# Performance work log

Measured on AMD Instinct MI355X. Metric: run time of the kernel, lower is better.

Reference implementation:

```python
import jax, jax.numpy as jnp
import numpy as np

N = 65536      # nodes (256x256 grid)
E = 1048576    # edges (avg degree 16)
T_IN = 10      # TIME_STEPS_IN
L = 64         # LATENT_DIMS
MID = 128      # LATENT_DIMS * MLP_RATIO
GD = 2         # grid dims


def _lin_init(key, fan_in, fan_out):
    kw, kb = jax.random.split(key)
    s = 1.0 / np.sqrt(fan_in)
    W = jax.random.uniform(kw, (fan_in, fan_out), jnp.float32, -s, s)
    b = jax.random.uniform(kb, (fan_out,), jnp.float32, -s, s)
    return W, b


def setup_inputs() -> dict:
    key = jax.random.key(0)
    ks = jax.random.split(key, 10)
    x = jax.random.normal(ks[0], (N, T_IN), jnp.float32)
    grid = jax.random.uniform(ks[1], (N, GD), jnp.float32)
    edge_index = jax.random.randint(ks[2], (2, E), 0, N, jnp.int64)
    W_proj1, b_proj1 = _lin_init(ks[3], T_IN + GD, MID)
    W_proj2, b_proj2 = _lin_init(ks[4], MID, L)
    Wk, bk = _lin_init(ks[5], 2 * L + 2 * GD + 1, L)   # K edge MLP (single linear)
    Ww, bw = _lin_init(ks[6], L, L)                     # W node MLP (single linear)
    W_dec1, b_dec1 = _lin_init(ks[7], L, MID)
    W_dec2, b_dec2 = _lin_init(ks[8], MID, 1)
    return {"x": x, "grid": grid, "edge_index": edge_index,
            "W_proj1": W_proj1, "b_proj1": b_proj1, "W_proj2": W_proj2, "b_proj2": b_proj2,
            "Wk": Wk, "bk": bk, "Ww": Ww, "bw": bw,
            "W_dec1": W_dec1, "b_dec1": b_dec1, "W_dec2": W_dec2, "b_dec2": b_dec2}


def _gelu(x):
    return jax.nn.gelu(x, approximate=False)  # torch F.gelu default = exact erf


def reference(x, grid, edge_index, W_proj1, b_proj1, W_proj2, b_proj2,
              Wk, bk, Ww, bw, W_dec1, b_dec1, W_dec2, b_dec2):
    # project: cat(x, grid) -> Linear -> GELU -> Linear
    h = jnp.concatenate([x, grid], axis=-1)               # [N, T_IN+2]
    h = _gelu(h @ W_proj1 + b_proj1) @ W_proj2 + b_proj2  # [N, L]

    # message passing block (PyG source_to_target: j = row 0, i = row 1)
    src = edge_index[0]
    dst = edge_index[1]
    x_j = h[src]                                          # [E, L]
    x_i = h[dst]                                          # [E, L]
    g_j = grid[src]                                       # [E, 2]
    g_i = grid[dst]                                       # [E, 2]
    dist = jnp.sqrt(jnp.sum(jnp.square(g_i - g_j), axis=-1, keepdims=True))  # [E, 1]
    ef = jnp.concatenate([dist, g_i, g_j, x_i, x_j], axis=-1)  # [E, 2L+5]
    msg = ef @ Wk + bk                                    # [E, L]
    aggr = jax.ops.segment_sum(msg, dst, num_segments=N)  # [N, L]
    h = _gelu(h @ Ww + bw + aggr)                         # update

    # decode: Linear -> GELU -> Linear
    out = _gelu(h @ W_dec1 + b_dec1) @ W_dec2 + b_dec2    # [N, 1]
    return out
```

## Files before the change

### kernel.cpp

```cpp
#include <hip/hip_runtime.h>
#include <hip/hip_fp16.h>

static __device__ __forceinline__ float gelu(float x) {
    return 0.5f * x * (1.0f + erff(x * 0.70710678118654752f));
}

#define CAPR 32

typedef _Float16 v8h __attribute__((ext_vector_type(8)));
typedef float    v4f __attribute__((ext_vector_type(4)));
union F8 { uint4 u; v8h v; _Float16 f[8]; };

static __device__ __forceinline__ void acc8(float* a, uint4 u) {
    float2 f0 = __half22float2(*(__half2*)&u.x);
    float2 f1 = __half22float2(*(__half2*)&u.y);
    float2 f2 = __half22float2(*(__half2*)&u.z);
    float2 f3 = __half22float2(*(__half2*)&u.w);
    a[0] += f0.x; a[1] += f0.y; a[2] += f1.x; a[3] += f1.y;
    a[4] += f2.x; a[5] += f2.y; a[6] += f3.x; a[7] += f3.y;
}

static __device__ __forceinline__ uint4 pack8(const float* v) {
    __half2 p0 = __floats2half2_rn(v[0], v[1]);
    __half2 p1 = __floats2half2_rn(v[2], v[3]);
    __half2 p2 = __floats2half2_rn(v[4], v[5]);
    __half2 p3 = __floats2half2_rn(v[6], v[7]);
    uint4 u;
    u.x = *(unsigned*)&p0; u.y = *(unsigned*)&p1;
    u.z = *(unsigned*)&p2; u.w = *(unsigned*)&p3;
    return u;
}

__global__ void __launch_bounds__(256, 1)
k_enc_scat(const float* __restrict__ x,
           const float* __restrict__ grid,
           const float* __restrict__ W1,
           const float* __restrict__ b1,
           const float* __restrict__ W2,
           const float* __restrict__ b2,
           const int* __restrict__ ei, int* __restrict__ cnt,
           int* __restrict__ ssrc,
           __half* __restrict__ h16, int N, int E, int scatB)
{
    __shared__ uint4 tabW1[512];
    __shared__ uint4 tabW2[1024];
    __shared__ __half wmids[4 * 16 * 136];
    int tid = threadIdx.x;

    if ((int)blockIdx.x < scatB) {
        int e4 = blockIdx.x * 256 + tid;
        const int4* s4 = (const int4*)ei;
        const int4* d4 = (const int4*)(ei + E);
        int4 s = s4[e4];
        int4 d = d4[e4];
        int p;
        p = atomicAdd(&cnt[(d.x << 1) + 0], 1); if (p < CAPR) ssrc[((size_t)d.x << 6) + p] = s.x;
        p = atomicAdd(&cnt[(d.y << 1) + 1], 1); if (p < CAPR) ssrc[((size_t)d.y << 6) + 32 + p] = s.y;
        p = atomicAdd(&cnt[(d.z << 1) + 0], 1); if (p < CAPR) ssrc[((size_t)d.z << 6) + p] = s.z;
        p = atomicAdd(&cnt[(d.w << 1) + 1], 1); if (p < CAPR) ssrc[((size_t)d.w << 6) + 32 + p] = s.w;
        return;
    }

    int eb = blockIdx.x - scatB;
    for (int idx = tid; idx < 512; idx += 256) {
        int lane = idx & 63, nt = idx >> 6;
        int col = nt * 16 + (lane & 15);
        int k0 = (lane >> 4) << 3;
        F8 f;
#pragma unroll
        for (int j = 0; j < 8; j++)
            f.f[j] = (k0 + j < 12) ? (_Float16)W1[(k0 + j) * 128 + col] : (_Float16)0.f;
        tabW1[idx] = f.u;
    }
    for (int idx = tid; idx < 1024; idx += 256) {
        int lane = idx & 63, nt = (idx >> 6) & 3, kc = idx >> 8;
        int col = nt * 16 + (lane & 15);
        int k0 = kc * 32 + ((lane >> 4) << 3);
        F8 f;
#pragma unroll
        for (int j = 0; j < 8; j++) f.f[j] = (_Float16)W2[(k0 + j) * 64 + col];
        tabW2[idx] = f.u;
    }
    __syncthreads();

    int lane = tid & 63, wave = tid >> 6;
    int m = lane & 15, quad = lane >> 4;
    __half* wm = &wmids[wave * 16 * 136];

    for (int t = 0; t < 2; t++) {
        int tile = eb * 8 + wave * 2 + t;
        int base = tile * 16;
        int n = base + m;
        F8 a1;
#pragma unroll
        for (int j = 0; j < 8; j++) a1.f[j] = (_Float16)0.f;
        if (quad == 0) {
            float2 x0 = *(const float2*)&x[(size_t)n * 10 + 0];
            float2 x1 = *(const float2*)&x[(size_t)n * 10 + 2];
            float2 x2 = *(const float2*)&x[(size_t)n * 10 + 4];
            float2 x3 = *(const float2*)&x[(size_t)n * 10 + 6];
            a1.f[0] = (_Float16)x0.x; a1.f[1] = (_Float16)x0.y;
            a1.f[2] = (_Float16)x1.x; a1.f[3] = (_Float16)x1.y;
            a1.f[4] = (_Float16)x2.x; a1.f[5] = (_Float16)x2.y;
            a1.f[6] = (_Float16)x3.x; a1.f[7] = (_Float16)x3.y;
        } else if (quad == 1) {
            float2 x4 = *(const float2*)&x[(size_t)n * 10 + 8];
            float2 g  = *(const float2*)&grid[(size_t)n * 2];
            a1.f[0] = (_Float16)x4.x; a1.f[1] = (_Float16)x4.y;
            a1.f[2] = (_Float16)g.x;  a1.f[3] = (_Float16)g.y;
        }
#pragma unroll
        for (int nt = 0; nt < 8; nt++) {
            int col = nt * 16 + m;
            float b = b1[col];
            v4f acc = {b, b, b, b};
            F8 bf; bf.u = tabW1[nt * 64 + lane];
            acc = __builtin_amdgcn_mfma_f32_16x16x32_f16(a1.v, bf.v, acc, 0, 0, 0);
#pragma unroll
            for (int reg = 0; reg < 4; reg++)
                wm[(quad * 4 + reg) * 136 + col] = __float2half(gelu(acc[reg]));
        }
        __syncthreads();

        F8 a2[4];
#pragma unroll
        for (int kc = 0; kc < 4; kc++)
            a2[kc].u = *(const uint4*)&wm[m * 136 + kc * 32 + quad * 8];
#pragma unroll
        for (int nt = 0; nt < 4; nt++) {
            int col = nt * 16 + m;
            float b = b2[col];
            v4f acc = {b, b, b, b};
#pragma unroll
            for (int kc = 0; kc < 4; kc++) {
                F8 bf; bf.u = tabW2[kc * 256 + nt * 64 + lane];
                acc = __builtin_amdgcn_mfma_f32_16x16x32_f16(a2[kc].v, bf.v, acc, 0, 0, 0);
            }
#pragma unroll
            for (int reg = 0; reg < 4; reg++)
                h16[(size_t)(base + quad * 4 + reg) * 64 + col] = __float2half(acc[reg]);
        }
        __syncthreads();
    }
}

__global__ void k_gather(const __half* __restrict__ h16,
                         const float* __restrict__ grid,
                         const int* __restrict__ ssrc, const int* __restrict__ cnt,
                         __half* __restrict__ sum_h16, float* __restrict__ sum_g,
                         float* __restrict__ sum_d, int N)
{
    int tid = blockIdx.x * blockDim.x + threadIdx.x;
    int n = tid >> 3;
    int l = tid & 7;
    if (n >= N) return;
    int2 cv = *(const int2*)&cnt[n << 1];
    const uint4* h8 = (const uint4*)h16;
    float a[8] = {0,0,0,0,0,0,0,0};
    float sgx = 0.f, sgy = 0.f, sd = 0.f;
    float gix = grid[2 * n], giy = grid[2 * n + 1];
#pragma unroll
    for (int r = 0; r < 2; r++) {
        int dg = min((r == 0) ? cv.x : cv.y, CAPR);
        const int* sr = ssrc + ((size_t)n << 6) + (r << 5);
        for (int i = 0; i < dg; i += 4) {
            int4 s = *(const int4*)&sr[i];
            int rem = dg - i;
            if (rem < 4) {
                if (rem <= 1) s.y = s.x;
                if (rem <= 2) s.z = s.x;
                s.w = (rem <= 3) ? s.x : s.w;
            }
            uint4 u0 = h8[(size_t)s.x * 8 + l];
            uint4 u1 = h8[(size_t)s.y * 8 + l];
            uint4 u2 = h8[(size_t)s.z * 8 + l];
            uint4 u3 = h8[(size_t)s.w * 8 + l];
            acc8(a, u0);
            if (rem > 1) acc8(a, u1);
            if (rem > 2) acc8(a, u2);
            if (rem > 3) acc8(a, u3);
            if (l < 4 && i + l < dg) {
                int sj = (l == 0) ? s.x : (l == 1) ? s.y : (l == 2) ? s.z : s.w;
                float2 g = *(const float2*)&grid[2 * sj];
                float dx = gix - g.x, dy = giy - g.y;
                sd += sqrtf(dx * dx + dy * dy);
                sgx += g.x; sgy += g.y;
            }
        }
    }
    sd  += __shfl_xor(sd, 1);  sd  += __shfl_xor(sd, 2);  sd  += __shfl_xor(sd, 4);
    sgx += __shfl_xor(sgx, 1); sgx += __shfl_xor(sgx, 2); sgx += __shfl_xor(sgx, 4);
    sgy += __shfl_xor(sgy, 1); sgy += __shfl_xor(sgy, 2); sgy += __shfl_xor(sgy, 4);
    ((uint4*)(sum_h16 + (size_t)n * 64))[l] = pack8(a);
    if (l == 0) { sum_d[n] = sd; sum_g[2 * n] = sgx; sum_g[2 * n + 1] = sgy; }
}

__global__ void __launch_bounds__(256, 1)
k_updec(const __half* __restrict__ h16, const __half* __restrict__ sum_h16,
        const float* __restrict__ sum_g, const float* __restrict__ sum_d,
        const int* __restrict__ cnt, const float* __restrict__ grid,
        const float* __restrict__ Wk, const float* __restrict__ bk,
        const float* __restrict__ Ww, const float* __restrict__ bw,
        const float* __restrict__ Wd1, const float* __restrict__ bd1,
        const float* __restrict__ Wd2, const float* __restrict__ bd2,
        float* __restrict__ out, int N)
{
    __shared__ uint4 tabW[512];
    __shared__ uint4 tabC[512];
    __shared__ uint4 tabD[512];
    __shared__ uint4 tabV[256];
    __shared__ uint4 tabE[1024];
    __shared__ __half h2t[4 * 16 * 72];
    int tid = threadIdx.x;

    for (int idx = tid; idx < 512; idx += 256) {
        int lane = idx & 63, nt = (idx >> 6) & 3, kc = idx >> 8;
        int col = nt * 16 + (lane & 15);
        int kr  = kc * 32 + ((lane >> 4) << 3);
        F8 fw, fc, fd;
#pragma unroll
        for (int j = 0; j < 8; j++) {
            fw.f[j] = (_Float16)Ww[(kr + j) * 64 + col];
            fc.f[j] = (_Float16)Wk[(size_t)(5 + kr + j) * 64 + col];
            fd.f[j] = (_Float16)Wk[(size_t)(69 + kr + j) * 64 + col];
        }
        tabW[idx] = fw.u; tabC[idx] = fc.u; tabD[idx] = fd.u;
    }
    if (tid < 256) {
        int lane = tid & 63, nt = tid >> 6;
        int col = nt * 16 + (lane & 15);
        F8 fv;
#pragma unroll
        for (int j = 0; j < 8; j++) fv.f[j] = (_Float16)0.f;
        if ((lane >> 4) == 0) {
            fv.f[0] = (_Float16)bw[col];
            fv.f[1] = (_Float16)bk[col];
            fv.f[2] = (_Float16)Wk[col];
            fv.f[3] = (_Float16)Wk[64 + col];
            fv.f[4] = (_Float16)Wk[128 + col];
            fv.f[5] = (_Float16)Wk[192 + col];
            fv.f[6] = (_Float16)Wk[256 + col];
        }
        tabV[tid] = fv.u;
    }
    for (int idx = tid; idx < 1024; idx += 256) {
        int lane = idx & 63, nt = (idx >> 6) & 7, kc = idx >> 9;
        int col = nt * 16 + (lane & 15);
        int kr  = kc * 32 + ((lane >> 4) << 3);
        F8 f;
#pragma unroll
        for (int j = 0; j < 8; j++) f.f[j] = (_Float16)Wd1[(kr + j) * 128 + col];
        tabE[idx] = f.u;
    }
    __syncthreads();

    int lane = tid & 63, wave = tid >> 6;
    int m = lane & 15, quad = lane >> 4;
    const uint4* h8 = (const uint4*)h16;
    const uint4* s8 = (const uint4*)sum_h16;
    __half* wt = &h2t[wave * 16 * 72];
    float bd2v = bd2[0];

    for (int t = 0; t < 2; t++) {
        int tile = blockIdx.x * 8 + wave * 2 + t;
        int base = tile * 16;
        int n = base + m;
        int2 cv = *(const int2*)&cnt[n << 1];
        float deg = (float)(min(cv.x, CAPR) + min(cv.y, CAPR));
        float sd  = sum_d[n];
        float sgx = sum_g[2 * n], sgy = sum_g[2 * n + 1];
        float gix = grid[2 * n] * deg, giy = grid[2 * n + 1] * deg;

        F8 ah0, ah1, as0, as1, ahd0, ahd1, au;
        ah0.u = h8[(size_t)n * 8 + quad];
        ah1.u = h8[(size_t)n * 8 + 4 + quad];
        as0.u = s8[(size_t)n * 8 + quad];
        as1.u = s8[(size_t)n * 8 + 4 + quad];
        _Float16 dh = (_Float16)deg;
#pragma unroll
        for (int j = 0; j < 8; j++) { ahd0.f[j] = ah0.f[j] * dh; ahd1.f[j] = ah1.f[j] * dh; }
        float z = (quad == 0) ? 1.f : 0.f;
        au.f[0] = (_Float16)z;          au.f[1] = (_Float16)(deg * z);
        au.f[2] = (_Float16)(sd * z);   au.f[3] = (_Float16)(gix * z);
        au.f[4] = (_Float16)(giy * z);  au.f[5] = (_Float16)(sgx * z);
        au.f[6] = (_Float16)(sgy * z);  au.f[7] = (_Float16)0.f;

#pragma unroll
        for (int nt = 0; nt < 4; nt++) {
            F8 bv, bw0, bw1, bc0, bc1, bd0, bd1f;
            bv.u  = tabV[nt * 64 + lane];
            bw0.u = tabW[nt * 64 + lane];       bw1.u = tabW[256 + nt * 64 + lane];
            bc0.u = tabC[nt * 64 + lane];       bc1.u = tabC[256 + nt * 64 + lane];
            bd0.u = tabD[nt * 64 + lane];       bd1f.u = tabD[256 + nt * 64 + lane];
            v4f acc = {0.f, 0.f, 0.f, 0.f};
            acc = __builtin_amdgcn_mfma_f32_16x16x32_f16(au.v,   bv.v,   acc, 0, 0, 0);
            acc = __builtin_amdgcn_mfma_f32_16x16x32_f16(ah0.v,  bw0.v,  acc, 0, 0, 0);
            acc = __builtin_amdgcn_mfma_f32_16x16x32_f16(ah1.v,  bw1.v,  acc, 0, 0, 0);
            acc = __builtin_amdgcn_mfma_f32_16x16x32_f16(ahd0.v, bc0.v,  acc, 0, 0, 0);
            acc = __builtin_amdgcn_mfma_f32_16x16x32_f16(ahd1.v, bc1.v,  acc, 0, 0, 0);
            acc = __builtin_amdgcn_mfma_f32_16x16x32_f16(as0.v,  bd0.v,  acc, 0, 0, 0);
            acc = __builtin_amdgcn_mfma_f32_16x16x32_f16(as1.v,  bd1f.v, acc, 0, 0, 0);
#pragma unroll
            for (int reg = 0; reg < 4; reg++)
                wt[(quad * 4 + reg) * 72 + m + 16 * nt] = __float2half(gelu(acc[reg]));
        }
        __syncthreads();

        F8 dh0, dh1;
        dh0.u = *(const uint4*)&wt[m * 72 + quad * 8];
        dh1.u = *(const uint4*)&wt[m * 72 + 32 + quad * 8];
        float p[4] = {0.f, 0.f, 0.f, 0.f};
#pragma unroll
        for (int nt = 0; nt < 8; nt++) {
            int col = m + 16 * nt;
            float b = bd1[col];
            float w2 = Wd2[col];
            F8 b0, b1;
            b0.u = tabE[nt * 64 + lane];
            b1.u = tabE[512 + nt * 64 + lane];
            v4f acc = {b, b, b, b};
            acc = __builtin_amdgcn_mfma_f32_16x16x32_f16(dh0.v, b0.v, acc, 0, 0, 0);
            acc = __builtin_amdgcn_mfma_f32_16x16x32_f16(dh1.v, b1.v, acc, 0, 0, 0);
#pragma unroll
            for (int reg = 0; reg < 4; reg++) p[reg] += gelu(acc[reg]) * w2;
        }
#pragma unroll
        for (int reg = 0; reg < 4; reg++) {
            p[reg] += __shfl_xor(p[reg], 1);
            p[reg] += __shfl_xor(p[reg], 2);
            p[reg] += __shfl_xor(p[reg], 4);
            p[reg] += __shfl_xor(p[reg], 8);
        }
        if (m == 0) {
#pragma unroll
            for (int reg = 0; reg < 4; reg++)
                out[base + quad * 4 + reg] = p[reg] + bd2v;
        }
        __syncthreads();
    }
}

extern "C" void kernel_launch(void* const* d_in, const int* in_sizes, int n_in,
                              void* d_out, int out_size, void* d_ws, size_t ws_size,
                              hipStream_t stream)
{
    const float* x    = (const float*)d_in[0];
    const float* grid = (const float*)d_in[1];
    const int*   ei   = (const int*)d_in[2];
    const float* W1   = (const float*)d_in[3];
    const float* b1   = (const float*)d_in[4];
    const float* W2   = (const float*)d_in[5];
    const float* b2   = (const float*)d_in[6];
    const float* Wk   = (const float*)d_in[7];
    const float* bk   = (const float*)d_in[8];
    const float* Ww   = (const float*)d_in[9];
    const float* bw   = (const float*)d_in[10];
    const float* Wd1  = (const float*)d_in[11];
    const float* bd1  = (const float*)d_in[12];
    const float* Wd2  = (const float*)d_in[13];
    const float* bd2  = (const float*)d_in[14];
    float* out = (float*)d_out;

    int N = in_sizes[0] / 10;
    int E = in_sizes[2] / 2;

    char* ws = (char*)d_ws;
    size_t o_h16  = 0;
    size_t o_sh16 = o_h16  + (size_t)N * 64 * 2;
    size_t o_sumg = o_sh16 + (size_t)N * 64 * 2;
    size_t o_sumd = o_sumg + (size_t)N * 2 * 4;
    size_t o_cnt  = o_sumd + (size_t)N * 4;
    size_t o_ssrc = o_cnt  + (size_t)N * 2 * 4;

    __half* h16     = (__half*)(ws + o_h16);
    __half* sum_h16 = (__half*)(ws + o_sh16);
    float* sum_g = (float*)(ws + o_sumg);
    float* sum_d = (float*)(ws + o_sumd);
    int*   cnt   = (int*)  (ws + o_cnt);
    int*   ssrc  = (int*)  (ws + o_ssrc);

    hipMemsetAsync(cnt, 0, (size_t)N * 2 * 4, stream);

    int scatB = E / (256 * 4);
    int encB  = (N / 16) / 8;
    k_enc_scat<<<dim3(scatB + encB), dim3(256), 0, stream>>>(x, grid, W1, b1, W2, b2,
                                                             ei, cnt, ssrc, h16, N, E, scatB);
    k_gather<<<dim3((N * 8 + 255) / 256), dim3(256), 0, stream>>>(h16, grid, ssrc, cnt,
                                                                   sum_h16, sum_g, sum_d, N);
    int tiles = N / 16;
    k_updec<<<dim3(tiles / 8), dim3(256), 0, stream>>>(h16, sum_h16, sum_g, sum_d, cnt,
                                                       grid, Wk, bk, Ww, bw,
                                                       Wd1, bd1, Wd2, bd2, out, N);
}
```

Baseline: 211.0 us.

## Fuse neighbor gather into update/decode kernel via shared-memory tiles

Moves the per-node neighbor aggregation (feature sums, grid sums, distance sums) into the update/decode kernel. Each wave now gathers its own 16-node tile into LDS instead of writing the sums to global workspace and reading them back in a separate launch. This removes one kernel launch and the global round trip of the aggregated features. The cost is that the gather now runs at the fused kernel's low occupancy (launch_bounds 256,1, large LDS use), which may hurt latency hiding for the random gathers.

Result: slower. 224.3 us (+6.3%).

```diff
diff --git a/kernel.cpp b/kernel.cpp
--- a/kernel.cpp
+++ b/kernel.cpp
@@ -144,73 +144,24 @@
     }
 }
 
-__global__ void k_gather(const __half* __restrict__ h16,
-                         const float* __restrict__ grid,
-                         const int* __restrict__ ssrc, const int* __restrict__ cnt,
-                         __half* __restrict__ sum_h16, float* __restrict__ sum_g,
-                         float* __restrict__ sum_d, int N)
-{
-    int tid = blockIdx.x * blockDim.x + threadIdx.x;
-    int n = tid >> 3;
-    int l = tid & 7;
-    if (n >= N) return;
-    int2 cv = *(const int2*)&cnt[n << 1];
-    const uint4* h8 = (const uint4*)h16;
-    float a[8] = {0,0,0,0,0,0,0,0};
-    float sgx = 0.f, sgy = 0.f, sd = 0.f;
-    float gix = grid[2 * n], giy = grid[2 * n + 1];
-#pragma unroll
-    for (int r = 0; r < 2; r++) {
-        int dg = min((r == 0) ? cv.x : cv.y, CAPR);
-        const int* sr = ssrc + ((size_t)n << 6) + (r << 5);
-        for (int i = 0; i < dg; i += 4) {
-            int4 s = *(const int4*)&sr[i];
-            int rem = dg - i;
-            if (rem < 4) {
-                if (rem <= 1) s.y = s.x;
-                if (rem <= 2) s.z = s.x;
-                s.w = (rem <= 3) ? s.x : s.w;
-            }
-            uint4 u0 = h8[(size_t)s.x * 8 + l];
-            uint4 u1 = h8[(size_t)s.y * 8 + l];
-            uint4 u2 = h8[(size_t)s.z * 8 + l];
-            uint4 u3 = h8[(size_t)s.w * 8 + l];
-            acc8(a, u0);
-            if (rem > 1) acc8(a, u1);
-            if (rem > 2) acc8(a, u2);
-            if (rem > 3) acc8(a, u3);
-            if (l < 4 && i + l < dg) {
-                int sj = (l == 0) ? s.x : (l == 1) ? s.y : (l == 2) ? s.z : s.w;
-                float2 g = *(const float2*)&grid[2 * sj];
-                float dx = gix - g.x, dy = giy - g.y;
-                sd += sqrtf(dx * dx + dy * dy);
-                sgx += g.x; sgy += g.y;
-            }
-        }
-    }
-    sd  += __shfl_xor(sd, 1);  sd  += __shfl_xor(sd, 2);  sd  += __shfl_xor(sd, 4);
-    sgx += __shfl_xor(sgx, 1); sgx += __shfl_xor(sgx, 2); sgx += __shfl_xor(sgx, 4);
-    sgy += __shfl_xor(sgy, 1); sgy += __shfl_xor(sgy, 2); sgy += __shfl_xor(sgy, 4);
-    ((uint4*)(sum_h16 + (size_t)n * 64))[l] = pack8(a);
-    if (l == 0) { sum_d[n] = sd; sum_g[2 * n] = sgx; sum_g[2 * n + 1] = sgy; }
-}
-
 __global__ void __launch_bounds__(256, 1)
-k_updec(const __half* __restrict__ h16, const __half* __restrict__ sum_h16,
-        const float* __restrict__ sum_g, const float* __restrict__ sum_d,
-        const int* __restrict__ cnt, const float* __restrict__ grid,
-        const float* __restrict__ Wk, const float* __restrict__ bk,
-        const float* __restrict__ Ww, const float* __restrict__ bw,
-        const float* __restrict__ Wd1, const float* __restrict__ bd1,
-        const float* __restrict__ Wd2, const float* __restrict__ bd2,
-        float* __restrict__ out, int N)
+k_gat_updec(const __half* __restrict__ h16,
+            const float* __restrict__ grid,
+            const int* __restrict__ ssrc, const int* __restrict__ cnt,
+            const float* __restrict__ Wk, const float* __restrict__ bk,
+            const float* __restrict__ Ww, const float* __restrict__ bw,
+            const float* __restrict__ Wd1, const float* __restrict__ bd1,
+            const float* __restrict__ Wd2, const float* __restrict__ bd2,
+            float* __restrict__ out, int N)
 {
     __shared__ uint4 tabW[512];
     __shared__ uint4 tabC[512];
     __shared__ uint4 tabD[512];
     __shared__ uint4 tabV[256];
     __shared__ uint4 tabE[1024];
-    __shared__ __half h2t[4 * 16 * 72];
+    __shared__ __half stile[4][16 * 72];
+    __shared__ __half h2t[4][16 * 72];
+    __shared__ float  stats[4][16][4];
     int tid = threadIdx.x;
 
     for (int idx = tid; idx < 512; idx += 256) {
@@ -257,25 +208,74 @@
     int lane = tid & 63, wave = tid >> 6;
     int m = lane & 15, quad = lane >> 4;
     const uint4* h8 = (const uint4*)h16;
-    const uint4* s8 = (const uint4*)sum_h16;
-    __half* wt = &h2t[wave * 16 * 72];
     float bd2v = bd2[0];
 
     for (int t = 0; t < 2; t++) {
         int tile = blockIdx.x * 8 + wave * 2 + t;
         int base = tile * 16;
+
+#pragma unroll
+        for (int p = 0; p < 2; p++) {
+            int ng = (lane >> 3) + p * 8;
+            int l  = lane & 7;
+            int n  = base + ng;
+            int2 cv = *(const int2*)&cnt[n << 1];
+            float a[8] = {0,0,0,0,0,0,0,0};
+            float sgx = 0.f, sgy = 0.f, sd = 0.f;
+            float gix = grid[2 * n], giy = grid[2 * n + 1];
+#pragma unroll
+            for (int r = 0; r < 2; r++) {
+                int dg = min((r == 0) ? cv.x : cv.y, CAPR);
+                const int* sr = ssrc + ((size_t)n << 6) + (r << 5);
+                for (int i = 0; i < dg; i += 4) {
+                    int4 s = *(const int4*)&sr[i];
+                    int rem = dg - i;
+                    if (rem < 4) {
+                        if (rem <= 1) s.y = s.x;
+                        if (rem <= 2) s.z = s.x;
+                        s.w = (rem <= 3) ? s.x : s.w;
+                    }
+                    uint4 u0 = h8[(size_t)s.x * 8 + l];
+                    uint4 u1 = h8[(size_t)s.y * 8 + l];
+                    uint4 u2 = h8[(size_t)s.z * 8 + l];
+                    uint4 u3 = h8[(size_t)s.w * 8 + l];
+                    acc8(a, u0);
+                    if (rem > 1) acc8(a, u1);
+                    if (rem > 2) acc8(a, u2);
+                    if (rem > 3) acc8(a, u3);
+                    if (l < 4 && i + l < dg) {
+                        int sj = (l == 0) ? s.x : (l == 1) ? s.y : (l == 2) ? s.z : s.w;
+                        float2 g = *(const float2*)&grid[2 * sj];
+                        float dx = gix - g.x, dy = giy - g.y;
+                        sd += sqrtf(dx * dx + dy * dy);
+                        sgx += g.x; sgy += g.y;
+                    }
+                }
+            }
+            sd  += __shfl_xor(sd, 1);  sd  += __shfl_xor(sd, 2);  sd  += __shfl_xor(sd, 4);
+            sgx += __shfl_xor(sgx, 1); sgx += __shfl_xor(sgx, 2); sgx += __shfl_xor(sgx, 4);
+            sgy += __shfl_xor(sgy, 1); sgy += __shfl_xor(sgy, 2); sgy += __shfl_xor(sgy, 4);
+            *(uint4*)&stile[wave][ng * 72 + l * 8] = pack8(a);
+            if (l == 0) {
+                stats[wave][ng][0] = sd;
+                stats[wave][ng][1] = sgx;
+                stats[wave][ng][2] = sgy;
+            }
+        }
+        __syncthreads();
+
         int n = base + m;
         int2 cv = *(const int2*)&cnt[n << 1];
         float deg = (float)(min(cv.x, CAPR) + min(cv.y, CAPR));
-        float sd  = sum_d[n];
-        float sgx = sum_g[2 * n], sgy = sum_g[2 * n + 1];
+        float sd  = stats[wave][m][0];
+        float sgx = stats[wave][m][1], sgy = stats[wave][m][2];
         float gix = grid[2 * n] * deg, giy = grid[2 * n + 1] * deg;
 
         F8 ah0, ah1, as0, as1, ahd0, ahd1, au;
         ah0.u = h8[(size_t)n * 8 + quad];
         ah1.u = h8[(size_t)n * 8 + 4 + quad];
-        as0.u = s8[(size_t)n * 8 + quad];
-        as1.u = s8[(size_t)n * 8 + 4 + quad];
+        as0.u = *(const uint4*)&stile[wave][m * 72 + quad * 8];
+        as1.u = *(const uint4*)&stile[wave][m * 72 + 32 + quad * 8];
         _Float16 dh = (_Float16)deg;
 #pragma unroll
         for (int j = 0; j < 8; j++) { ahd0.f[j] = ah0.f[j] * dh; ahd1.f[j] = ah1.f[j] * dh; }
@@ -302,13 +302,13 @@
             acc = __builtin_amdgcn_mfma_f32_16x16x32_f16(as1.v,  bd1f.v, acc, 0, 0, 0);
 #pragma unroll
             for (int reg = 0; reg < 4; reg++)
-                wt[(quad * 4 + reg) * 72 + m + 16 * nt] = __float2half(gelu(acc[reg]));
+                h2t[wave][(quad * 4 + reg) * 72 + m + 16 * nt] = __float2half(gelu(acc[reg]));
         }
         __syncthreads();
 
         F8 dh0, dh1;
-        dh0.u = *(const uint4*)&wt[m * 72 + quad * 8];
-        dh1.u = *(const uint4*)&wt[m * 72 + 32 + quad * 8];
+        dh0.u = *(const uint4*)&h2t[wave][m * 72 + quad * 8];
+        dh1.u = *(const uint4*)&h2t[wave][m * 72 + 32 + quad * 8];
         float p[4] = {0.f, 0.f, 0.f, 0.f};
 #pragma unroll
         for (int nt = 0; nt < 8; nt++) {
@@ -366,18 +366,12 @@
 
     char* ws = (char*)d_ws;
     size_t o_h16  = 0;
-    size_t o_sh16 = o_h16  + (size_t)N * 64 * 2;
-    size_t o_sumg = o_sh16 + (size_t)N * 64 * 2;
-    size_t o_sumd = o_sumg + (size_t)N * 2 * 4;
-    size_t o_cnt  = o_sumd + (size_t)N * 4;
-    size_t o_ssrc = o_cnt  + (size_t)N * 2 * 4;
-
-    __half* h16     = (__half*)(ws + o_h16);
-    __half* sum_h16 = (__half*)(ws + o_sh16);
-    float* sum_g = (float*)(ws + o_sumg);
-    float* sum_d = (float*)(ws + o_sumd);
-    int*   cnt   = (int*)  (ws + o_cnt);
-    int*   ssrc  = (int*)  (ws + o_ssrc);
+    size_t o_cnt  = o_h16 + (size_t)N * 64 * 2;
+    size_t o_ssrc = o_cnt + (size_t)N * 2 * 4;
+
+    __half* h16 = (__half*)(ws + o_h16);
+    int*    cnt = (int*)  (ws + o_cnt);
+    int*    ssrc = (int*) (ws + o_ssrc);
 
     hipMemsetAsync(cnt, 0, (size_t)N * 2 * 4, stream);
 
@@ -385,10 +379,8 @@
     int encB  = (N / 16) / 8;
     k_enc_scat<<<dim3(scatB + encB), dim3(256), 0, stream>>>(x, grid, W1, b1, W2, b2,
                                                              ei, cnt, ssrc, h16, N, E, scatB);
-    k_gather<<<dim3((N * 8 + 255) / 256), dim3(256), 0, stream>>>(h16, grid, ssrc, cnt,
-                                                                   sum_h16, sum_g, sum_d, N);
     int tiles = N / 16;
-    k_updec<<<dim3(tiles / 8), dim3(256), 0, stream>>>(h16, sum_h16, sum_g, sum_d, cnt,
-                                                       grid, Wk, bk, Ww, bw,
-                                                       Wd1, bd1, Wd2, bd2, out, N);
-}
+    k_gat_updec<<<dim3(tiles / 8), dim3(256), 0, stream>>>(h16, grid, ssrc, cnt,
+                                                           Wk, bk, Ww, bw,
+                                                           Wd1, bd1, Wd2, bd2, out, N);
+}
```
